# Optimization experiments

Hardware: AMD Instinct MI355X
Metric: run time of the kernel (lower is better)

Reference implementation:

```python
import jax, jax.numpy as jnp
import numpy as np
import math

N, MA, NFS, K, RC = 4, 256, 128, 8, 5.0
HID, OUT = 256, 32


def setup_inputs() -> dict:
    key = jax.random.key(0)
    ks = jax.random.split(key, 9)
    z = jax.random.randint(ks[0], (N, MA), 0, 10)
    r = jax.random.normal(ks[1], (N, MA, 3), dtype=jnp.float32) * 3.0
    h = jax.random.normal(ks[2], (N, MA, NFS), dtype=jnp.float32)
    Wa = jax.random.normal(ks[3], (2 * NFS, 1), dtype=jnp.float32) * 0.05
    ba = jnp.zeros((1,), dtype=jnp.float32)
    Wp1 = jax.random.normal(ks[4], (2 * NFS, HID), dtype=jnp.float32) * 0.05
    bp1 = jnp.zeros((HID,), dtype=jnp.float32)
    Wp2 = jax.random.normal(ks[5], (HID, OUT), dtype=jnp.float32) * 0.05
    bp2 = jnp.zeros((OUT,), dtype=jnp.float32)
    return {"z": z, "r": r, "h": h, "Wa": Wa, "ba": ba,
            "Wp1": Wp1, "bp1": bp1, "Wp2": Wp2, "bp2": bp2}


def reference(z, r, h, Wa, ba, Wp1, bp1, Wp2, bp2):
    n, ma = z.shape
    nfs = h.shape[2]
    # distance vectors dv[b,i,j] = r[b,j] - r[b,i]  -> [n, ma, ma, 3]
    dv = r[:, None, :, :] - r[:, :, None, :]
    d = jnp.linalg.norm(dv, axis=3)                       # [n, ma, ma]
    eye = jnp.eye(ma, dtype=jnp.float32)
    # cosine cutoff, zeroed on the diagonal
    cf = 0.5 * (jnp.cos(math.pi * jnp.minimum(d, RC) / RC) + 1.0)
    cf = (cf - eye[None])[..., None]                      # [n, ma, ma, 1]
    # pair validity mask (z > -1 marks real atoms), diagonal removed
    m = (z > -1).astype(jnp.float32)                      # [n, ma]
    mask = m[:, None, :] * m[:, :, None] - eye[None]
    mask = jnp.clip(mask, 0.0)[..., None]                 # [n, ma, ma, 1]
    cf = cf * mask
    # pairwise feature tensor u = [h_i, h_j * cf]         # [n, ma, ma, 2*nfs]
    u1 = jnp.broadcast_to(h[:, :, None, :], (n, ma, ma, nfs))
    u2 = h[:, None, :, :] * cf
    u = jnp.concatenate([u1, u2], axis=3)
    # exp attention, masked, normalized over neighbor axis (dim 2)
    g = (u @ Wa + ba) * mask                              # [n, ma, ma, 1]
    g = jnp.exp(g) - (1.0 - mask)
    attention = g / jnp.clip(g.sum(axis=2, keepdims=True), 1e-8)
    # top-k neighbors per query atom
    att, index = jax.lax.top_k(attention[..., 0], K)      # [n, ma, K]
    att = att[..., None]
    # gather neighbor features and distance vectors
    h2 = jnp.take_along_axis(h[:, None, :, :], index[..., None], axis=2)  # [n, ma, K, nfs]
    h1 = jnp.broadcast_to(h[:, :, None, :], (n, ma, K, nfs))
    uk = jnp.concatenate([h1, h2], axis=3) * att          # [n, ma, K, 2*nfs]
    dvk = jnp.take_along_axis(dv, index[..., None], axis=2)               # [n, ma, K, 3]
    dvk = dvk / jnp.clip(jnp.linalg.norm(dvk, axis=3, keepdims=True), 1e-4)
    dvk = dvk[:, :, :, None, :]                           # [n, ma, K, 1, 3]
    # pool MLP then cross with unit direction vectors
    c = jax.nn.silu(uk @ Wp1 + bp1) @ Wp2 + bp2           # [n, ma, K, OUT]
    c = c[..., None] * dvk                                # [n, ma, K, OUT, 3]
    return (z, r, c)
```

## Files before the change

kernel.cpp:

```cpp
#include <hip/hip_runtime.h>
#include <hip/hip_bf16.h>
#include <math.h>

#define NB 4
#define MA 256
#define NFS 128
#define KSEL 8
#define HID 256
#define NOUT 32
#define RCUT 5.0f
#define PI_F 3.14159265358979323846f

__global__ __launch_bounds__(256) void prep_kernel(
    const int* __restrict__ z, const float* __restrict__ r,
    const float* __restrict__ h, const float* __restrict__ Wa,
    const float* __restrict__ Wp1,
    float* __restrict__ out,
    float* __restrict__ a1, float* __restrict__ a2,
    float* __restrict__ P, float* __restrict__ Q) {
  const int b = blockIdx.x;
  const int half = b & 1;
  const int rg = b >> 1;
  const int r0 = 4 * rg;
  const int t = threadIdx.x;
  const int wave = t >> 6, lane = t & 63;
  const int c = t & 63, fq = t >> 6;

  __shared__ __align__(16) float hsh[4][NFS];
  __shared__ __align__(16) float psum[4][4][HID];

  ((float2*)hsh)[t] = ((const float2*)(h + (size_t)r0 * NFS))[t];
  __syncthreads();

  if (half == 0) {
    const float h0 = hsh[wave][lane], h1 = hsh[wave][lane + 64];
    float p1 = h0 * Wa[lane]       + h1 * Wa[lane + 64];
    float p2 = h0 * Wa[NFS + lane] + h1 * Wa[NFS + lane + 64];
#pragma unroll
    for (int off = 32; off > 0; off >>= 1) {
      p1 += __shfl_down(p1, off);
      p2 += __shfl_down(p2, off);
    }
    if (lane == 0) { a1[r0 + wave] = p1; a2[r0 + wave] = p2; }
    if (t < 4)  out[r0 + t] = (float)z[r0 + t];
    if (t < 12) out[NB * MA + r0 * 3 + t] = r[r0 * 3 + t];
  }

  const float* __restrict__ Wbase = Wp1 + (size_t)(half ? NFS : 0) * HID;
  float4 acc[4] = {make_float4(0,0,0,0), make_float4(0,0,0,0),
                   make_float4(0,0,0,0), make_float4(0,0,0,0)};
#pragma unroll 4
  for (int ff = 0; ff < 32; ++ff) {
    const int f = fq * 32 + ff;
    const float4 w = *(const float4*)&Wbase[(size_t)f * HID + 4 * c];
#pragma unroll
    for (int rr = 0; rr < 4; ++rr) {
      const float hv = hsh[rr][f];
      acc[rr].x = fmaf(hv, w.x, acc[rr].x);
      acc[rr].y = fmaf(hv, w.y, acc[rr].y);
      acc[rr].z = fmaf(hv, w.z, acc[rr].z);
      acc[rr].w = fmaf(hv, w.w, acc[rr].w);
    }
  }
#pragma unroll
  for (int rr = 0; rr < 4; ++rr) *(float4*)&psum[fq][rr][4 * c] = acc[rr];
  __syncthreads();

  {
    const int r2 = t >> 6, c2 = t & 63;
    float4 s = *(const float4*)&psum[0][r2][4 * c2];
#pragma unroll
    for (int q = 1; q < 4; ++q) {
      const float4 p = *(const float4*)&psum[q][r2][4 * c2];
      s.x += p.x; s.y += p.y; s.z += p.z; s.w += p.w;
    }
    float* dst = (half ? Q : P) + (size_t)(r0 + r2) * HID + 4 * c2;
    *(float4*)dst = s;
  }
}

__global__ __launch_bounds__(256) void main_kernel(
    const int* __restrict__ z, const float* __restrict__ r,
    const float* __restrict__ a1g, const float* __restrict__ a2g,
    const float* __restrict__ ba,
    const float* __restrict__ Pg, const float* __restrict__ Qg,
    const float* __restrict__ bp1,
    const float* __restrict__ Wp2g, const float* __restrict__ bp2,
    float* __restrict__ out) {
  const int row = blockIdx.x;
  const int n = row >> 8;
  const int i = row & 255;
  const int tid = threadIdx.x;
  const int lane = tid & 63;

  __shared__ float gsh[MA];
  __shared__ __align__(16) float hid_sh[KSEL][HID];
  __shared__ float psum2[8][KSEL][NOUT];

  const int l2o = tid & 31;
  const int l2c = tid >> 5;
  float wreg[32];
#pragma unroll
  for (int j = 0; j < 32; ++j) wreg[j] = Wp2g[(size_t)(32 * l2c + j) * NOUT + l2o];

  const float rix = r[row * 3 + 0], riy = r[row * 3 + 1], riz = r[row * 3 + 2];
  {
    const int jg = n * MA + tid;
    const float dx = r[jg * 3 + 0] - rix;
    const float dy = r[jg * 3 + 1] - riy;
    const float dz = r[jg * 3 + 2] - riz;
    const float d = sqrtf(dx * dx + dy * dy + dz * dz);
    const int mi = (z[row] > -1) ? 1 : 0;
    const int mj = (z[jg] > -1) ? 1 : 0;
    const int mask = max(mi * mj - ((tid == i) ? 1 : 0), 0);
    float g = 0.0f;
    if (mask) {
      const float cf = 0.5f * (__cosf(PI_F * fminf(d, RCUT) / RCUT) + 1.0f);
      g = __expf(a1g[row] + cf * a2g[jg] + ba[0]);
    }
    gsh[tid] = g;
  }
  __syncthreads();

  float att[KSEL];
  int   idx[KSEL];
  {
    float v0 = gsh[lane];
    float v1 = gsh[lane + 64];
    float v2 = gsh[lane + 128];
    float v3 = gsh[lane + 192];
    float s = (v0 + v1) + (v2 + v3);
#pragma unroll
    for (int off = 32; off > 0; off >>= 1) s += __shfl_xor(s, off);
    const float rden = 1.0f / fmaxf(s, 1e-8f);
#pragma unroll
    for (int k = 0; k < KSEL; k++) {
      float bv = v0; int bi = lane;
      if (v1 > bv) { bv = v1; bi = lane + 64; }
      if (v2 > bv) { bv = v2; bi = lane + 128; }
      if (v3 > bv) { bv = v3; bi = lane + 192; }
#pragma unroll
      for (int off = 32; off > 0; off >>= 1) {
        const float ov = __shfl_xor(bv, off);
        const int oi = __shfl_xor(bi, off);
        if (ov > bv || (ov == bv && oi < bi)) { bv = ov; bi = oi; }
      }
      att[k] = bv * rden;
      idx[k] = __builtin_amdgcn_readfirstlane(bi);
      const int slot = bi >> 6, who = bi & 63;
      if (lane == who) {
        if (slot == 0) v0 = -1.0f;
        else if (slot == 1) v1 = -1.0f;
        else if (slot == 2) v2 = -1.0f;
        else v3 = -1.0f;
      }
    }
  }

  {
    const float pi = Pg[(size_t)row * HID + tid];
    const float bb = bp1[tid];
#pragma unroll
    for (int k = 0; k < KSEL; k++) {
      const float q = Qg[(size_t)(n * MA + idx[k]) * HID + tid];
      const float x = att[k] * (pi + q) + bb;
      hid_sh[k][tid] = x / (1.0f + __expf(-x));
    }
  }
  __syncthreads();

  {
    float acc[KSEL];
#pragma unroll
    for (int k = 0; k < KSEL; ++k) acc[k] = 0.0f;
#pragma unroll
    for (int k = 0; k < KSEL; ++k) {
      const float4* __restrict__ hrow = (const float4*)&hid_sh[k][32 * l2c];
#pragma unroll
      for (int j4 = 0; j4 < 8; ++j4) {
        const float4 hv = hrow[j4];
        acc[k] = fmaf(hv.x, wreg[4 * j4 + 0],
                 fmaf(hv.y, wreg[4 * j4 + 1],
                 fmaf(hv.z, wreg[4 * j4 + 2],
                 fmaf(hv.w, wreg[4 * j4 + 3], acc[k]))));
      }
    }
#pragma unroll
    for (int k = 0; k < KSEL; ++k) psum2[l2c][k][l2o] = acc[k];
  }
  __syncthreads();

  {
    const int k2 = tid >> 5;
    const int o = tid & 31;
    float s = bp2[o];
#pragma unroll
    for (int cc = 0; cc < 8; ++cc) s += psum2[cc][k2][o];
    const int jg = n * MA + idx[k2];
    const float dx = r[jg * 3 + 0] - rix;
    const float dy = r[jg * 3 + 1] - riy;
    const float dz = r[jg * 3 + 2] - riz;
    const float nrm = fmaxf(sqrtf(dx * dx + dy * dy + dz * dz), 1e-4f);
    float* cb = out + NB * MA + NB * MA * 3 +
                ((size_t)row * KSEL + k2) * (NOUT * 3) + o * 3;
    cb[0] = s * (dx / nrm);
    cb[1] = s * (dy / nrm);
    cb[2] = s * (dz / nrm);
  }
}

extern "C" void kernel_launch(void* const* d_in, const int* in_sizes, int n_in,
                              void* d_out, int out_size, void* d_ws, size_t ws_size,
                              hipStream_t stream) {
  const int*   z   = (const int*)d_in[0];
  const float* r   = (const float*)d_in[1];
  const float* h   = (const float*)d_in[2];
  const float* Wa  = (const float*)d_in[3];
  const float* ba  = (const float*)d_in[4];
  const float* Wp1 = (const float*)d_in[5];
  const float* bp1 = (const float*)d_in[6];
  const float* Wp2 = (const float*)d_in[7];
  const float* bp2 = (const float*)d_in[8];
  float* out = (float*)d_out;

  float* a1 = (float*)d_ws;
  float* a2 = a1 + NB * MA;
  float* P  = a2 + NB * MA;
  float* Q  = P + (size_t)NB * MA * HID;

  prep_kernel<<<2 * NB * MA / 4, 256, 0, stream>>>(z, r, h, Wa, Wp1, out, a1, a2, P, Q);
  main_kernel<<<NB * MA, 256, 0, stream>>>(z, r, a1, a2, ba, P, Q, bp1, Wp2, bp2, out);
}
```

Measured before the change: 22.91 us.

## Stage Wp2 through LDS, hoist P/bias loads, use fast rcp/sqrt intrinsics

Wp2 is now copied into shared memory with coalesced float4 loads, and each thread reads its register slice from LDS instead of making 32 strided global loads. The P-row and bias loads are moved before the first barrier so their latency overlaps the attention computation. IEEE divide and sqrt are replaced with the hardware rcp/sqrt intrinsics, and the dynamic idx[k2] register index becomes a select tree. The cost is 32 KB of extra LDS per block, which can reduce occupancy, plus slightly lower numeric precision.

Result: slower. 27.74 us (+21.1%).

```diff
diff --git a/kernel.cpp b/kernel.cpp
--- a/kernel.cpp
+++ b/kernel.cpp
@@ -10,6 +10,9 @@
 #define NOUT 32
 #define RCUT 5.0f
 #define PI_F 3.14159265358979323846f
+
+__device__ __forceinline__ float frcp(float x) { return __builtin_amdgcn_rcpf(x); }
+__device__ __forceinline__ float fsqrt(float x) { return __builtin_amdgcn_sqrtf(x); }
 
 __global__ __launch_bounds__(256) void prep_kernel(
     const int* __restrict__ z, const float* __restrict__ r,
@@ -94,14 +97,16 @@
   const int lane = tid & 63;
 
   __shared__ float gsh[MA];
+  __shared__ __align__(16) float wsh[HID * NOUT];
   __shared__ __align__(16) float hid_sh[KSEL][HID];
   __shared__ float psum2[8][KSEL][NOUT];
 
-  const int l2o = tid & 31;
-  const int l2c = tid >> 5;
-  float wreg[32];
-#pragma unroll
-  for (int j = 0; j < 32; ++j) wreg[j] = Wp2g[(size_t)(32 * l2c + j) * NOUT + l2o];
+  {
+    const float4* __restrict__ src = (const float4*)Wp2g;
+    float4* dst = (float4*)wsh;
+#pragma unroll
+    for (int j = 0; j < 8; ++j) dst[tid + 256 * j] = src[tid + 256 * j];
+  }
 
   const float rix = r[row * 3 + 0], riy = r[row * 3 + 1], riz = r[row * 3 + 2];
   {
@@ -109,7 +114,7 @@
     const float dx = r[jg * 3 + 0] - rix;
     const float dy = r[jg * 3 + 1] - riy;
     const float dz = r[jg * 3 + 2] - riz;
-    const float d = sqrtf(dx * dx + dy * dy + dz * dz);
+    const float d = fsqrt(dx * dx + dy * dy + dz * dz);
     const int mi = (z[row] > -1) ? 1 : 0;
     const int mj = (z[jg] > -1) ? 1 : 0;
     const int mask = max(mi * mj - ((tid == i) ? 1 : 0), 0);
@@ -120,7 +125,15 @@
     }
     gsh[tid] = g;
   }
-  __syncthreads();
+  const float pi_h = Pg[(size_t)row * HID + tid];
+  const float bb_h = bp1[tid];
+  __syncthreads();
+
+  const int l2o = tid & 31;
+  const int l2c = tid >> 5;
+  float wreg[32];
+#pragma unroll
+  for (int j = 0; j < 32; ++j) wreg[j] = wsh[(32 * l2c + j) * NOUT + l2o];
 
   float att[KSEL];
   int   idx[KSEL];
@@ -132,7 +145,7 @@
     float s = (v0 + v1) + (v2 + v3);
 #pragma unroll
     for (int off = 32; off > 0; off >>= 1) s += __shfl_xor(s, off);
-    const float rden = 1.0f / fmaxf(s, 1e-8f);
+    const float rden = frcp(fmaxf(s, 1e-8f));
 #pragma unroll
     for (int k = 0; k < KSEL; k++) {
       float bv = v0; int bi = lane;
@@ -158,13 +171,11 @@
   }
 
   {
-    const float pi = Pg[(size_t)row * HID + tid];
-    const float bb = bp1[tid];
 #pragma unroll
     for (int k = 0; k < KSEL; k++) {
       const float q = Qg[(size_t)(n * MA + idx[k]) * HID + tid];
-      const float x = att[k] * (pi + q) + bb;
-      hid_sh[k][tid] = x / (1.0f + __expf(-x));
+      const float x = att[k] * (pi_h + q) + bb_h;
+      hid_sh[k][tid] = x * frcp(1.0f + __expf(-x));
     }
   }
   __syncthreads();
@@ -196,16 +207,23 @@
     float s = bp2[o];
 #pragma unroll
     for (int cc = 0; cc < 8; ++cc) s += psum2[cc][k2][o];
-    const int jg = n * MA + idx[k2];
+    const int j01 = (k2 & 1) ? idx[1] : idx[0];
+    const int j23 = (k2 & 1) ? idx[3] : idx[2];
+    const int j45 = (k2 & 1) ? idx[5] : idx[4];
+    const int j67 = (k2 & 1) ? idx[7] : idx[6];
+    const int j03 = (k2 & 2) ? j23 : j01;
+    const int j47 = (k2 & 2) ? j67 : j45;
+    const int jsel = (k2 & 4) ? j47 : j03;
+    const int jg = n * MA + jsel;
     const float dx = r[jg * 3 + 0] - rix;
     const float dy = r[jg * 3 + 1] - riy;
     const float dz = r[jg * 3 + 2] - riz;
-    const float nrm = fmaxf(sqrtf(dx * dx + dy * dy + dz * dz), 1e-4f);
+    const float rn = frcp(fmaxf(fsqrt(dx * dx + dy * dy + dz * dz), 1e-4f));
     float* cb = out + NB * MA + NB * MA * 3 +
                 ((size_t)row * KSEL + k2) * (NOUT * 3) + o * 3;
-    cb[0] = s * (dx / nrm);
-    cb[1] = s * (dy / nrm);
-    cb[2] = s * (dz / nrm);
+    cb[0] = s * (dx * rn);
+    cb[1] = s * (dy * rn);
+    cb[2] = s * (dz * rn);
   }
 }
 
```
